# Optimization experiments

Measured on AMD Instinct MI355X. Metric: run time of the kernel, lower is better.

## Reference

```python
import jax, jax.numpy as jnp
from jax import lax
import numpy as np

EPS = 1e-5
NEG_SLOPE = 0.2

# 4D conv via lax.conv_general_dilated (supports arbitrary spatial rank)
_DN = ('NCABXY', 'OIABXY', 'NCABXY')  # N,C + 4 spatial dims

def conv4d(x, w):
    # x: (N, Cin, S1, S2, H, W); w: (Cout, Cin, 3, 3, 3, 3); padding=1, stride=1
    return lax.conv_general_dilated(
        x, w,
        window_strides=(1, 1, 1, 1),
        padding=[(1, 1)] * 4,
        dimension_numbers=_DN,
    )

def instance_norm4d(x):
    # normalize per (n, c) over all 4 spatial dims; no affine (PyTorch default)
    mean = jnp.mean(x, axis=(2, 3, 4, 5), keepdims=True)
    var = jnp.var(x, axis=(2, 3, 4, 5), keepdims=True)
    return (x - mean) * lax.rsqrt(var + EPS)

def leaky_relu(x):
    return jnp.where(x >= 0, x, NEG_SLOPE * x)

def setup_inputs() -> dict:
    key = jax.random.key(0)
    k0, k1, k2 = jax.random.split(key, 3)
    image = jax.random.normal(k0, (1, 16, 8, 16, 64, 64), dtype=jnp.float32)
    # He-ish init scale for kernel 3^4
    w1 = jax.random.normal(k1, (32, 16, 3, 3, 3, 3), dtype=jnp.float32) * 0.03
    w2 = jax.random.normal(k2, (32, 32, 3, 3, 3, 3), dtype=jnp.float32) * 0.02
    return {"image": image, "w1": w1, "w2": w2}

def reference(image, w1, w2):
    x = leaky_relu(instance_norm4d(conv4d(image, w1)))
    x = leaky_relu(instance_norm4d(conv4d(x, w2)))
    return x
```

## Files before the change

### kernel.cpp

```cpp
#include <hip/hip_runtime.h>

#define D1 8
#define D2 16
#define HH 64
#define WW 64
#define SPATIAL (D1*D2*HH*WW)
#define EPS 1e-5f
#define NEG 0.2f

typedef unsigned short u16;
typedef __attribute__((ext_vector_type(8))) short s16x8;
typedef __attribute__((ext_vector_type(8))) unsigned short u16x8;
typedef __attribute__((ext_vector_type(4))) unsigned short u16x4;
typedef __attribute__((ext_vector_type(4))) float f32x4;

__device__ __forceinline__ u16 f2bf(float f) {
    unsigned int u = __builtin_bit_cast(unsigned int, f);
    return (u16)((u + 0x7FFFu + ((u >> 16) & 1u)) >> 16);
}
__device__ __forceinline__ float bf2f(u16 u) {
    unsigned int v = ((unsigned int)u) << 16;
    return __builtin_bit_cast(float, v);
}
__device__ __forceinline__ float leaky(float x) {
    return x >= 0.f ? x : NEG * x;
}

__device__ __forceinline__ void decode_block(int flat, int& a, int& b, int& h0) {
    int xcd  = flat & 7;
    int slot = flat >> 3;
    int ht   = slot & 7;
    int b0   = (slot >> 3) & 1;
    a        = (slot >> 4) & 7;
    b        = xcd * 2 + b0;
    h0       = ht * 8;
}

__global__ __launch_bounds__(256)
void prep(const float* __restrict__ img, const float* __restrict__ w1,
          const float* __restrict__ w2, u16* __restrict__ imgT,
          u16* __restrict__ w1t, u16* __restrict__ w2t, float* __restrict__ st)
{
    const int bid = blockIdx.x;
    const int tid = threadIdx.x;
    if (bid < 2048) {
        int p = bid * 256 + tid;
        u16 r[16];
        #pragma unroll
        for (int c = 0; c < 16; ++c)
            r[c] = f2bf(img[(size_t)c * SPATIAL + p]);
        u16x8 lo, hi;
        #pragma unroll
        for (int j = 0; j < 8; ++j) { lo[j] = r[j]; hi[j] = r[8 + j]; }
        u16x8* dst = (u16x8*)(imgT + (size_t)p * 16);
        dst[0] = lo;
        dst[1] = hi;
    } else if (bid < 2264) {
        int i = (bid - 2048) * 256 + tid;
        if (i >= 55296) return;
        int k    = i & 31;
        int co   = (i >> 5) & 31;
        int grp  = (i >> 10) & 1;
        int rest = i >> 11;
        int dh   = rest % 3;
        int p    = rest / 3;
        int da = p / 3, db = p % 3;
        float v = 0.f;
        if (grp == 0) {
            int dw = k >> 4, ci = k & 15;
            v = w1[((((co * 16 + ci) * 3 + da) * 3 + db) * 3 + dh) * 3 + dw];
        } else if (k < 16) {
            v = w1[((((co * 16 + k) * 3 + da) * 3 + db) * 3 + dh) * 3 + 2];
        }
        w1t[i] = f2bf(v);
    } else if (bid < 2588) {
        int i = (bid - 2264) * 256 + tid;
        if (i >= 82944) return;
        int ci = i & 31;
        int co = (i >> 5) & 31;
        int t  = (i >> 10) % 9;
        int p  = (i >> 10) / 9;
        int da = p / 3, db = p % 3, dh = t / 3, dw = t % 3;
        w2t[i] = f2bf(w2[((((co * 32 + ci) * 3 + da) * 3 + db) * 3 + dh) * 3 + dw]);
    } else {
        if (tid < 128) st[tid] = 0.f;
    }
}

#define C1_LDBF(DST, BASE, GRP) { \
    _Pragma("unroll") \
    for (int dh_ = 0; dh_ < 3; ++dh_) { \
        const u16* wb_ = (BASE) + (dh_ * 2 + (GRP)) * 1024; \
        DST[dh_][0] = *(const s16x8*)(wb_ + m * 32 + kq * 8); \
        DST[dh_][1] = *(const s16x8*)(wb_ + (m + 16) * 32 + kq * 8); \
    } }

#define C1_MFMA(BF, CSHIFT) { \
    const int eb_ = (kq & 1) * 8; \
    _Pragma("unroll") \
    for (int x_ = 0; x_ < 10; ++x_) { \
        int pos_ = x_ * 66 + wseg + m + (CSHIFT); \
        s16x8 af_ = *(const s16x8*)&lds[pos_ * 24 + eb_]; \
        _Pragma("unroll") \
        for (int dh_ = 0; dh_ < 3; ++dh_) { \
            int i_ = x_ - dh_; \
            if (i_ >= 0 && i_ < 8) { \
                acc[i_][0] = __builtin_amdgcn_mfma_f32_16x16x32_bf16(af_, BF[dh_][0], acc[i_][0], 0, 0, 0); \
                acc[i_][1] = __builtin_amdgcn_mfma_f32_16x16x32_bf16(af_, BF[dh_][1], acc[i_][1], 0, 0, 0); \
            } \
        } \
    } }

#define C1_PF(K0, K1) { \
    _Pragma("unroll") \
    for (int k_ = (K0); k_ < (K1); ++k_) \
        if ((vmask >> k_) & 1) pf[k_] = *(const u16x8*)(srcn + gbase + k_ * 2048); }

__global__ __launch_bounds__(256, 3)
void conv1_mfma(const u16* __restrict__ xT, const u16* __restrict__ w1t,
                u16* __restrict__ y1, float* __restrict__ st1)
{
    __shared__ __align__(16) u16 lds[660 * 24];
    __shared__ float sred[64];

    const int tid = threadIdx.x;
    int a, b, h0;
    decode_block(blockIdx.x, a, b, h0);
    const int lane = tid & 63;
    const int wv   = tid >> 6;
    const int kq   = lane >> 4;
    const int m    = lane & 15;
    const int wseg = wv << 4;

    unsigned pm = 0;
    #pragma unroll
    for (int p = 0; p < 9; ++p) {
        int ap = a + p / 3 - 1, bp = b + p % 3 - 1;
        if (ap >= 0 && ap < D1 && bp >= 0 && bp < D2) pm |= 1u << p;
    }

    const int p0f  = tid >> 1, g = tid & 1;
    const int hi   = p0f >> 6;
    const int p0c  = p0f & 63;
    unsigned vmask = 0;
    #pragma unroll
    for (int k = 0; k < 5; ++k) {
        int h = h0 - 1 + 2 * k + hi;
        if (h >= 0 && h < HH) vmask |= 1u << k;
    }
    const int gbase = ((h0 - 1 + hi) * WW + p0c) * 16 + g * 8;
    const int lbase = (hi * 66 + p0c + 1) * 24 + g * 8;

    for (int e = tid; e < 660; e += 256) {
        int row = e / 66, col = e - row * 66;
        int h = h0 - 1 + row;
        if (col == 0 || col == 65 || h < 0 || h >= HH) {
            u16x8 z = (u16x8)0;
            *(u16x8*)&lds[e * 24]     = z;
            *(u16x8*)&lds[e * 24 + 8] = z;
        }
    }

    f32x4 acc[8][2];
    #pragma unroll
    for (int i = 0; i < 8; ++i)
        #pragma unroll
        for (int nt = 0; nt < 2; ++nt)
            acc[i][nt] = (f32x4)0.f;

    int p = 0;
    while (!((pm >> p) & 1)) ++p;

    s16x8 bfX[3][2], bfY[3][2];
    C1_LDBF(bfX, w1t + p * 6144, 0);

    u16x8 pf[5];
    {
        const u16* srcn = xT + (size_t)((a + p / 3 - 1) * D2 + (b + p % 3 - 1))
                             * (HH * WW * 16);
        C1_PF(0, 5);
    }

    while (p < 9) {
        int pn = p + 1;
        while (pn < 9 && !((pm >> pn) & 1)) ++pn;

        #pragma unroll
        for (int k = 0; k < 5; ++k)
            if ((vmask >> k) & 1) *(u16x8*)&lds[lbase + k * 3168] = pf[k];
        __syncthreads();

        const u16* srcn = nullptr;
        if (pn < 9)
            srcn = xT + (size_t)((a + pn / 3 - 1) * D2 + (b + pn % 3 - 1))
                      * (HH * WW * 16);

        const u16* wbase = w1t + p * 6144;

        C1_LDBF(bfY, wbase, 1);
        C1_MFMA(bfX, (kq >> 1));
        if (pn < 9) C1_PF(0, 5);

        C1_MFMA(bfY, 2);

        __syncthreads();
        if (pn < 9) C1_LDBF(bfX, w1t + pn * 6144, 0);
        p = pn;
    }

    if (tid < 64) sred[tid] = 0.f;
    __syncthreads();

    float s[2] = {0.f, 0.f}, s2[2] = {0.f, 0.f};
    const size_t plane_out = (size_t)(a * D2 + b) * (HH * WW);
    #pragma unroll
    for (int i = 0; i < 8; ++i) {
        int h  = h0 + i;
        int w0 = wseg + kq * 4;
        #pragma unroll
        for (int nt = 0; nt < 2; ++nt) {
            int co = m + nt * 16;
            #pragma unroll
            for (int reg = 0; reg < 4; ++reg) {
                float v = acc[i][nt][reg];
                s[nt]  += v;
                s2[nt] += v * v;
                y1[(plane_out + h * WW + (w0 + reg)) * 32 + co] = f2bf(v);
            }
        }
    }
    #pragma unroll
    for (int nt = 0; nt < 2; ++nt) {
        s[nt]  += __shfl_xor(s[nt], 16);  s[nt]  += __shfl_xor(s[nt], 32);
        s2[nt] += __shfl_xor(s2[nt], 16); s2[nt] += __shfl_xor(s2[nt], 32);
    }
    if (kq == 0) {
        atomicAdd(&sred[m * 2],            s[0]);
        atomicAdd(&sred[m * 2 + 1],        s2[0]);
        atomicAdd(&sred[(m + 16) * 2],     s[1]);
        atomicAdd(&sred[(m + 16) * 2 + 1], s2[1]);
    }
    __syncthreads();
    if (tid < 64) atomicAdd(&st1[tid], sred[tid]);
}

__global__ __launch_bounds__(256)
void norm1_kernel(u16* __restrict__ y1, const float* __restrict__ st1)
{
    const int tid = threadIdx.x;
    const int q   = tid & 3;
    const float invN = 1.f / (float)SPATIAL;
    float mean[8], scl[8];
    #pragma unroll
    for (int j = 0; j < 8; ++j) {
        int ci  = q * 8 + j;
        float mu = st1[ci * 2] * invN;
        float va = st1[ci * 2 + 1] * invN - mu * mu;
        mean[j] = mu;
        scl[j]  = rsqrtf(va + EPS);
    }
    #pragma unroll
    for (int j4 = 0; j4 < 4; ++j4) {
        size_t gidx = (size_t)blockIdx.x * 1024 + j4 * 256 + tid;
        u16x8* ptr = (u16x8*)(y1 + gidx * 8);
        u16x8 v = *ptr;
        u16x8 o;
        #pragma unroll
        for (int j = 0; j < 8; ++j)
            o[j] = f2bf(leaky((bf2f(v[j]) - mean[j]) * scl[j]));
        *ptr = o;
    }
}

#define C2_LDBF(DST, BASE, DW) { \
    _Pragma("unroll") \
    for (int dh_ = 0; dh_ < 3; ++dh_) { \
        const u16* wb_ = (BASE) + (dh_ * 3 + (DW)) * 1024; \
        DST[dh_][0] = *(const s16x8*)(wb_ + m * 32 + kq * 8); \
        DST[dh_][1] = *(const s16x8*)(wb_ + (m + 16) * 32 + kq * 8); \
    } }

#define C2_MFMA(BF, DW) { \
    _Pragma("unroll") \
    for (int x_ = 0; x_ < 10; ++x_) { \
        int pos_ = x_ * 66 + wseg + (DW) + m; \
        s16x8 af_ = *(const s16x8*)&lds[pos_ * 40 + kq * 8]; \
        _Pragma("unroll") \
        for (int dh_ = 0; dh_ < 3; ++dh_) { \
            int i_ = x_ - dh_; \
            if (i_ >= 0 && i_ < 8) { \
                acc[i_][0] = __builtin_amdgcn_mfma_f32_16x16x32_bf16(af_, BF[dh_][0], acc[i_][0], 0, 0, 0); \
                acc[i_][1] = __builtin_amdgcn_mfma_f32_16x16x32_bf16(af_, BF[dh_][1], acc[i_][1], 0, 0, 0); \
            } \
        } \
    } }

#define C2_PF(K0, K1) { \
    _Pragma("unroll") \
    for (int k_ = (K0); k_ < (K1); ++k_) \
        if ((vmask >> k_) & 1) pf[k_] = *(const u16x8*)(srcn + gbase + k_ * 2048); }

__global__ __launch_bounds__(256, 3)
void conv2_mfma(const u16* __restrict__ y1, const u16* __restrict__ w2t,
                u16* __restrict__ y2, float* __restrict__ st2)
{
    __shared__ __align__(16) u16 lds[660 * 40];
    __shared__ float sred[64];

    const int tid = threadIdx.x;
    int a, b, h0;
    decode_block(blockIdx.x, a, b, h0);
    const int lane = tid & 63;
    const int wv   = tid >> 6;
    const int kq   = lane >> 4;
    const int m    = lane & 15;
    const int wseg = wv << 4;

    unsigned pm = 0;
    #pragma unroll
    for (int p = 0; p < 9; ++p) {
        int ap = a + p / 3 - 1, bp = b + p % 3 - 1;
        if (ap >= 0 && ap < D1 && bp >= 0 && bp < D2) pm |= 1u << p;
    }

    const int p0 = tid >> 2, q = tid & 3;
    unsigned vmask = 0;
    #pragma unroll
    for (int k = 0; k < 10; ++k) {
        int h = h0 - 1 + k;
        if (h >= 0 && h < HH) vmask |= 1u << k;
    }
    const int gbase = ((h0 - 1) * WW + p0) * 32 + q * 8;
    const int lbase = (p0 + 1) * 40 + q * 8;

    for (int e = tid; e < 660; e += 256) {
        int row = e / 66, col = e - row * 66;
        int h = h0 - 1 + row;
        if (col == 0 || col == 65 || h < 0 || h >= HH) {
            u16x8 z = (u16x8)0;
            #pragma unroll
            for (int gg = 0; gg < 4; ++gg)
                *(u16x8*)&lds[e * 40 + gg * 8] = z;
        }
    }

    f32x4 acc[8][2];
    #pragma unroll
    for (int i = 0; i < 8; ++i)
        #pragma unroll
        for (int nt = 0; nt < 2; ++nt)
            acc[i][nt] = (f32x4)0.f;

    int p = 0;
    while (!((pm >> p) & 1)) ++p;

    s16x8 bfX[3][2], bfY[3][2];
    C2_LDBF(bfX, w2t + p * 9216, 0);

    u16x8 pf[10];
    {
        const u16* srcn = y1 + (size_t)((a + p / 3 - 1) * D2 + (b + p % 3 - 1))
                             * (HH * WW * 32);
        C2_PF(0, 10);
    }

    while (p < 9) {
        int pn = p + 1;
        while (pn < 9 && !((pm >> pn) & 1)) ++pn;

        #pragma unroll
        for (int k = 0; k < 10; ++k)
            if ((vmask >> k) & 1) *(u16x8*)&lds[lbase + k * 2640] = pf[k];
        __syncthreads();

        const u16* srcn = nullptr;
        if (pn < 9)
            srcn = y1 + (size_t)((a + pn / 3 - 1) * D2 + (b + pn % 3 - 1))
                      * (HH * WW * 32);

        const u16* wbase = w2t + p * 9216;

        C2_LDBF(bfY, wbase, 1);
        C2_MFMA(bfX, 0);
        if (pn < 9) C2_PF(0, 5);

        C2_LDBF(bfX, wbase, 2);
        C2_MFMA(bfY, 1);
        if (pn < 9) C2_PF(5, 10);

        C2_MFMA(bfX, 2);

        __syncthreads();
        if (pn < 9) C2_LDBF(bfX, w2t + pn * 9216, 0);
        p = pn;
    }

    if (tid < 64) sred[tid] = 0.f;
    __syncthreads();

    float s[2] = {0.f, 0.f}, s2[2] = {0.f, 0.f};
    #pragma unroll
    for (int i = 0; i < 8; ++i) {
        int h  = h0 + i;
        int w0 = wseg + kq * 4;
        #pragma unroll
        for (int nt = 0; nt < 2; ++nt) {
            int co = m + nt * 16;
            u16x4 pk;
            #pragma unroll
            for (int reg = 0; reg < 4; ++reg) {
                float v = acc[i][nt][reg];
                s[nt]  += v;
                s2[nt] += v * v;
                pk[reg] = f2bf(v);
            }
            size_t off = ((size_t)(co * D1 + a) * D2 + b) * (HH * WW) + h * WW + w0;
            *(u16x4*)(y2 + off) = pk;
        }
    }
    #pragma unroll
    for (int nt = 0; nt < 2; ++nt) {
        s[nt]  += __shfl_xor(s[nt], 16);  s[nt]  += __shfl_xor(s[nt], 32);
        s2[nt] += __shfl_xor(s2[nt], 16); s2[nt] += __shfl_xor(s2[nt], 32);
    }
    if (kq == 0) {
        atomicAdd(&sred[m * 2],            s[0]);
        atomicAdd(&sred[m * 2 + 1],        s2[0]);
        atomicAdd(&sred[(m + 16) * 2],     s[1]);
        atomicAdd(&sred[(m + 16) * 2 + 1], s2[1]);
    }
    __syncthreads();
    if (tid < 64) atomicAdd(&st2[tid], sred[tid]);
}

__global__ __launch_bounds__(256)
void norm2_kernel(const u16* __restrict__ y2, const float* __restrict__ st2,
                  float* __restrict__ out)
{
    size_t i4 = (size_t)blockIdx.x * 256 + threadIdx.x;
    int c = (int)(i4 >> 17);
    const float invN = 1.f / (float)SPATIAL;
    float mu = st2[c * 2] * invN;
    float va = st2[c * 2 + 1] * invN - mu * mu;
    float sc = rsqrtf(va + EPS);
    u16x4 v = *(const u16x4*)(y2 + i4 * 4);
    float4 o;
    o.x = leaky((bf2f(v[0]) - mu) * sc);
    o.y = leaky((bf2f(v[1]) - mu) * sc);
    o.z = leaky((bf2f(v[2]) - mu) * sc);
    o.w = leaky((bf2f(v[3]) - mu) * sc);
    *(float4*)(out + i4 * 4) = o;
}

extern "C" void kernel_launch(void* const* d_in, const int* in_sizes, int n_in,
                              void* d_out, int out_size, void* d_ws, size_t ws_size,
                              hipStream_t stream)
{
    const float* image = (const float*)d_in[0];
    const float* w1    = (const float*)d_in[1];
    const float* w2    = (const float*)d_in[2];
    float* out = (float*)d_out;

    u16*   imgT = (u16*)d_ws;
    u16*   y1   = (u16*)((char*)d_ws + 33554432);
    u16*   y2   = imgT;
    float* st   = (float*)((char*)d_ws + 67108864);
    float* st1  = st;
    float* st2  = st + 64;

    u16* w1t = (u16*)((char*)d_out + 66832384);
    u16* w2t = (u16*)((char*)d_out + 66942976);

    prep<<<2589, 256, 0, stream>>>(image, w1, w2, imgT, w1t, w2t, st);

    conv1_mfma<<<1024, 256, 0, stream>>>(imgT, w1t, y1, st1);
    norm1_kernel<<<2048, 256, 0, stream>>>(y1, st1);
    conv2_mfma<<<1024, 256, 0, stream>>>(y1, w2t, y2, st2);
    norm2_kernel<<<16384, 256, 0, stream>>>(y2, st2, out);
}
```

Measured before the change: 250.0 us.

## Fuse instance-norm1 and leaky ReLU into conv2 input prefetch

Removes the separate norm1 kernel, which read and rewrote the whole bf16 intermediate. conv2 now computes per-channel scale and shift from the first-layer statistics and normalizes each prefetched tile in registers before storing it to LDS. This avoids one full memory round trip and a launch. In exchange, the normalization is recomputed for every neighbor plane and halo row, adding ALU work and register pressure inside the pipelined conv loop.

```diff
diff --git a/kernel.cpp b/kernel.cpp
--- a/kernel.cpp
+++ b/kernel.cpp
@@ -244,34 +244,6 @@
     if (tid < 64) atomicAdd(&st1[tid], sred[tid]);
 }
 
-__global__ __launch_bounds__(256)
-void norm1_kernel(u16* __restrict__ y1, const float* __restrict__ st1)
-{
-    const int tid = threadIdx.x;
-    const int q   = tid & 3;
-    const float invN = 1.f / (float)SPATIAL;
-    float mean[8], scl[8];
-    #pragma unroll
-    for (int j = 0; j < 8; ++j) {
-        int ci  = q * 8 + j;
-        float mu = st1[ci * 2] * invN;
-        float va = st1[ci * 2 + 1] * invN - mu * mu;
-        mean[j] = mu;
-        scl[j]  = rsqrtf(va + EPS);
-    }
-    #pragma unroll
-    for (int j4 = 0; j4 < 4; ++j4) {
-        size_t gidx = (size_t)blockIdx.x * 1024 + j4 * 256 + tid;
-        u16x8* ptr = (u16x8*)(y1 + gidx * 8);
-        u16x8 v = *ptr;
-        u16x8 o;
-        #pragma unroll
-        for (int j = 0; j < 8; ++j)
-            o[j] = f2bf(leaky((bf2f(v[j]) - mean[j]) * scl[j]));
-        *ptr = o;
-    }
-}
-
 #define C2_LDBF(DST, BASE, DW) { \
     _Pragma("unroll") \
     for (int dh_ = 0; dh_ < 3; ++dh_) { \
@@ -300,9 +272,23 @@
     for (int k_ = (K0); k_ < (K1); ++k_) \
         if ((vmask >> k_) & 1) pf[k_] = *(const u16x8*)(srcn + gbase + k_ * 2048); }
 
+#define C2_NRM(K0, K1) { \
+    _Pragma("unroll") \
+    for (int k_ = (K0); k_ < (K1); ++k_) \
+        if ((vmask >> k_) & 1) { \
+            u16x8 v_ = pf[k_]; \
+            _Pragma("unroll") \
+            for (int j_ = 0; j_ < 8; ++j_) { \
+                float x_ = bf2f(v_[j_]) * scl8[j_] + bet8[j_]; \
+                v_[j_] = f2bf(leaky(x_)); \
+            } \
+            pf[k_] = v_; \
+        } }
+
 __global__ __launch_bounds__(256, 3)
 void conv2_mfma(const u16* __restrict__ y1, const u16* __restrict__ w2t,
-                u16* __restrict__ y2, float* __restrict__ st2)
+                u16* __restrict__ y2, const float* __restrict__ st1,
+                float* __restrict__ st2)
 {
     __shared__ __align__(16) u16 lds[660 * 40];
     __shared__ float sred[64];
@@ -332,6 +318,18 @@
     }
     const int gbase = ((h0 - 1) * WW + p0) * 32 + q * 8;
     const int lbase = (p0 + 1) * 40 + q * 8;
+
+    const float invN = 1.f / (float)SPATIAL;
+    float scl8[8], bet8[8];
+    #pragma unroll
+    for (int j = 0; j < 8; ++j) {
+        int ci = q * 8 + j;
+        float mu = st1[ci * 2] * invN;
+        float va = st1[ci * 2 + 1] * invN - mu * mu;
+        float sc = rsqrtf(va + EPS);
+        scl8[j] = sc;
+        bet8[j] = -mu * sc;
+    }
 
     for (int e = tid; e < 660; e += 256) {
         int row = e / 66, col = e - row * 66;
@@ -363,6 +361,7 @@
                              * (HH * WW * 32);
         C2_PF(0, 10);
     }
+    C2_NRM(0, 10);
 
     while (p < 9) {
         int pn = p + 1;
@@ -386,9 +385,10 @@
 
         C2_LDBF(bfX, wbase, 2);
         C2_MFMA(bfY, 1);
-        if (pn < 9) C2_PF(5, 10);
+        if (pn < 9) { C2_PF(5, 10); C2_NRM(0, 5); }
 
         C2_MFMA(bfX, 2);
+        if (pn < 9) C2_NRM(5, 10);
 
         __syncthreads();
         if (pn < 9) C2_LDBF(bfX, w2t + pn * 9216, 0);
@@ -474,7 +474,6 @@
     prep<<<2589, 256, 0, stream>>>(image, w1, w2, imgT, w1t, w2t, st);
 
     conv1_mfma<<<1024, 256, 0, stream>>>(imgT, w1t, y1, st1);
-    norm1_kernel<<<2048, 256, 0, stream>>>(y1, st1);
-    conv2_mfma<<<1024, 256, 0, stream>>>(y1, w2t, y2, st2);
+    conv2_mfma<<<1024, 256, 0, stream>>>(y1, w2t, y2, st1, st2);
     norm2_kernel<<<16384, 256, 0, stream>>>(y2, st2, out);
 }
```

Result: slower. 286.7 us (+14.7%).
